# Kernel tuning notes

Hardware: AMD Instinct MI355X
Metric: run time of the kernel (lower is better)

Reference implementation:

```python
import jax, jax.numpy as jnp
import numpy as np

B, TOPK, E, C, K = 64, 2, 16, 1024, 4096


def setup_inputs() -> dict:
    key = jax.random.key(0)
    k1, k2, k3, k4, k5, k6 = jax.random.split(key, 6)
    return {
        "activated": jax.random.normal(k1, (B, TOPK, K), dtype=jnp.float32),
        "expert_indices": jax.random.randint(k2, (B, TOPK), 0, E, dtype=jnp.int64)
        if jax.config.jax_enable_x64 else jax.random.randint(k2, (B, TOPK), 0, E, dtype=jnp.int32),
        "expert_weights": jax.random.uniform(k3, (B, TOPK), dtype=jnp.float32),
        "mlp2_weight": jax.random.normal(k4, (E, C, K), dtype=jnp.float32),
        "mlp2_bias": jax.random.normal(k5, (E, C), dtype=jnp.float32),
        "residual_x": jax.random.normal(k6, (B, C), dtype=jnp.float32),
    }


def reference(activated, expert_indices, expert_weights, mlp2_weight, mlp2_bias, residual_x):
    # Gather per-token expert weights/biases: w [B, topk, C, K], b [B, topk, C]
    w = mlp2_weight[expert_indices]
    b = mlp2_bias[expert_indices]
    # Batched matvec per (token, expert slot): t [B, topk, C]
    t = jnp.einsum("beck,bek->bec", w, activated) + b
    # Weighted combine over top-k expert slots, plus residual: [B, C]
    return residual_x + jnp.einsum("bec,be->bc", t, expert_weights)
```

## Files before the change

### kernel.cpp

```cpp
#include <hip/hip_runtime.h>

#define BB    64
#define TOPK  2
#define EE    16
#define CC    1024
#define KK    4096

constexpr int RPB = 8;
constexpr int P   = 16;
constexpr int NW  = KK / 4 / 64;

__global__ __launch_bounds__(256) void route_init(
    const int* __restrict__ idx, const float* __restrict__ ew,
    const float* __restrict__ bias, const float* __restrict__ resid,
    float* __restrict__ out, int* __restrict__ cnt, int* __restrict__ lists)
{
    if (blockIdx.x == 0) {
        __shared__ int scnt[EE];
        if (threadIdx.x < EE) scnt[threadIdx.x] = 0;
        __syncthreads();
        if (threadIdx.x < BB * TOPK) {
            int e = idx[threadIdx.x];
            int pos = atomicAdd(&scnt[e], 1);
            lists[e * 128 + pos] = threadIdx.x;
        }
        __syncthreads();
        if (threadIdx.x < EE) cnt[threadIdx.x] = scnt[threadIdx.x];
    } else {
        int i = (blockIdx.x - 1) * 256 + threadIdx.x;
        int b = i >> 10;
        int c = i & (CC - 1);
        float v = resid[i];
#pragma unroll
        for (int s = 0; s < TOPK; s++) {
            int e = idx[b * TOPK + s];
            v += ew[b * TOPK + s] * bias[e * CC + c];
        }
        out[i] = v;
    }
}

__global__ __launch_bounds__(256) void moe_mlp2(
    const float* __restrict__ act, const float* __restrict__ ew,
    const float* __restrict__ W, float* __restrict__ out,
    const int* __restrict__ cnt, const int* __restrict__ lists)
{
    const int e = blockIdx.x >> 7;
    const int n = cnt[e];
    if (n == 0) return;
    const int c0   = (blockIdx.x & 127) * RPB;
    const int lane = threadIdx.x & 63;
    const int wave = threadIdx.x >> 6;
    const float4* We0 = (const float4*)(W + (size_t)(e * CC + c0 + wave * 2) * KK);
    const float4* We1 = We0 + (KK / 4);

    for (int g = 0; g < n; g += P) {
        const int np = min(P, n - g);

        int aoff[P];
#pragma unroll
        for (int p = 0; p < P; p++)
            aoff[p] = (p < np) ? lists[e * 128 + g + p] * (KK * 4) : 0;

        float acc[2][P];
#pragma unroll
        for (int r = 0; r < 2; r++)
#pragma unroll
            for (int p = 0; p < P; p++) acc[r][p] = 0.f;

#pragma unroll 2
        for (int kw = 0; kw < NW; kw++) {
            const int fi = kw * 64 + lane;
            const float4 w0 = We0[fi];
            const float4 w1 = We1[fi];
            const char* abase = (const char*)act + ((size_t)fi << 4);
#pragma unroll
            for (int pc = 0; pc < P / 4; pc++) {
                if (pc * 4 < np) {
#pragma unroll
                    for (int j = 0; j < 4; j++) {
                        const int p = pc * 4 + j;
                        const float4 a = *(const float4*)(abase + aoff[p]);
                        acc[0][p] += w0.x * a.x + w0.y * a.y + w0.z * a.z + w0.w * a.w;
                        acc[1][p] += w1.x * a.x + w1.y * a.y + w1.z * a.z + w1.w * a.w;
                    }
                }
            }
        }

#pragma unroll
        for (int p = 0; p < P; p++) {
            if (p < np) {
                float v0 = acc[0][p];
                float v1 = acc[1][p];
#pragma unroll
                for (int off = 32; off > 0; off >>= 1) {
                    v0 += __shfl_down(v0, off, 64);
                    v1 += __shfl_down(v1, off, 64);
                }
                if (lane == 0) {
                    int pr = lists[e * 128 + g + p];
                    float w = ew[pr];
                    float* o = out + (pr >> 1) * CC + c0 + wave * 2;
                    atomicAdd(o + 0, w * v0);
                    atomicAdd(o + 1, w * v1);
                }
            }
        }
    }
}

extern "C" void kernel_launch(void* const* d_in, const int* in_sizes, int n_in,
                              void* d_out, int out_size, void* d_ws, size_t ws_size,
                              hipStream_t stream) {
    const float* act   = (const float*)d_in[0];
    const int*   idx   = (const int*)d_in[1];
    const float* ew    = (const float*)d_in[2];
    const float* W     = (const float*)d_in[3];
    const float* bias  = (const float*)d_in[4];
    const float* resid = (const float*)d_in[5];
    float* out = (float*)d_out;

    int* cnt   = (int*)d_ws;
    int* lists = (int*)d_ws + 64;

    route_init<<<1 + (BB * CC) / 256, 256, 0, stream>>>(
        idx, ew, bias, resid, out, cnt, lists);
    moe_mlp2<<<EE * (CC / RPB), 256, 0, stream>>>(
        act, ew, W, out, cnt, lists);
}
```

Before: 404.6 us.

## Process four rows per wave, split K across two blocks, use nontemporal weight loads

Each wave now computes four weight rows instead of two, so every activation float4 load is reused across twice as many rows. The K dimension is split in half across paired blocks, which keeps the same grid size while doubling rows per block. Weight loads use nontemporal hints because the weight stream is read once. In exchange, register pressure from a 4x16 accumulator array rises, and there are twice as many atomic adds into the output.

```diff
diff --git a/kernel.cpp b/kernel.cpp
--- a/kernel.cpp
+++ b/kernel.cpp
@@ -6,9 +6,13 @@
 #define CC    1024
 #define KK    4096
 
-constexpr int RPB = 8;
+constexpr int RPB = 16;
 constexpr int P   = 16;
-constexpr int NW  = KK / 4 / 64;
+constexpr int KS  = 2;
+constexpr int KH  = KK / KS;
+constexpr int NW  = KH / 4 / 64;
+
+typedef float v4f __attribute__((ext_vector_type(4)));
 
 __global__ __launch_bounds__(256) void route_init(
     const int* __restrict__ idx, const float* __restrict__ ew,
@@ -45,44 +49,56 @@
     const float* __restrict__ W, float* __restrict__ out,
     const int* __restrict__ cnt, const int* __restrict__ lists)
 {
-    const int e = blockIdx.x >> 7;
+    const int bid = blockIdx.x;
+    const int e = bid >> 7;
     const int n = cnt[e];
     if (n == 0) return;
-    const int c0   = (blockIdx.x & 127) * RPB;
+    const int ct = (bid >> 1) & 63;
+    const int ks = bid & 1;
+    const int c0   = ct * RPB;
     const int lane = threadIdx.x & 63;
     const int wave = threadIdx.x >> 6;
-    const float4* We0 = (const float4*)(W + (size_t)(e * CC + c0 + wave * 2) * KK);
-    const float4* We1 = We0 + (KK / 4);
+    const int row0 = c0 + wave * 4;
+    const v4f* __restrict__ Wb =
+        (const v4f*)(W + (size_t)(e * CC + row0) * KK + ks * KH);
+    const char* __restrict__ actb = (const char*)(act + ks * KH);
 
     for (int g = 0; g < n; g += P) {
         const int np = min(P, n - g);
 
         int aoff[P];
+        int pid[P];
 #pragma unroll
-        for (int p = 0; p < P; p++)
-            aoff[p] = (p < np) ? lists[e * 128 + g + p] * (KK * 4) : 0;
+        for (int p = 0; p < P; p++) {
+            pid[p]  = (p < np) ? lists[e * 128 + g + p] : 0;
+            aoff[p] = pid[p] * (KK * 4);
+        }
 
-        float acc[2][P];
+        float acc[4][P];
 #pragma unroll
-        for (int r = 0; r < 2; r++)
+        for (int r = 0; r < 4; r++)
 #pragma unroll
             for (int p = 0; p < P; p++) acc[r][p] = 0.f;
 
 #pragma unroll 2
         for (int kw = 0; kw < NW; kw++) {
             const int fi = kw * 64 + lane;
-            const float4 w0 = We0[fi];
-            const float4 w1 = We1[fi];
-            const char* abase = (const char*)act + ((size_t)fi << 4);
+            v4f w4[4];
+#pragma unroll
+            for (int r = 0; r < 4; r++)
+                w4[r] = __builtin_nontemporal_load(Wb + (size_t)r * (KK / 4) + fi);
+            const char* abase = actb + ((size_t)fi << 4);
 #pragma unroll
             for (int pc = 0; pc < P / 4; pc++) {
                 if (pc * 4 < np) {
 #pragma unroll
                     for (int j = 0; j < 4; j++) {
                         const int p = pc * 4 + j;
-                        const float4 a = *(const float4*)(abase + aoff[p]);
-                        acc[0][p] += w0.x * a.x + w0.y * a.y + w0.z * a.z + w0.w * a.w;
-                        acc[1][p] += w1.x * a.x + w1.y * a.y + w1.z * a.z + w1.w * a.w;
+                        const v4f a = *(const v4f*)(abase + aoff[p]);
+#pragma unroll
+                        for (int r = 0; r < 4; r++)
+                            acc[r][p] += w4[r].x * a.x + w4[r].y * a.y +
+                                         w4[r].z * a.z + w4[r].w * a.w;
                     }
                 }
             }
@@ -91,19 +107,23 @@
 #pragma unroll
         for (int p = 0; p < P; p++) {
             if (p < np) {
-                float v0 = acc[0][p];
-                float v1 = acc[1][p];
+                float v0 = acc[0][p], v1 = acc[1][p];
+                float v2 = acc[2][p], v3 = acc[3][p];
 #pragma unroll
                 for (int off = 32; off > 0; off >>= 1) {
                     v0 += __shfl_down(v0, off, 64);
                     v1 += __shfl_down(v1, off, 64);
+                    v2 += __shfl_down(v2, off, 64);
+                    v3 += __shfl_down(v3, off, 64);
                 }
                 if (lane == 0) {
-                    int pr = lists[e * 128 + g + p];
+                    int pr = pid[p];
                     float w = ew[pr];
-                    float* o = out + (pr >> 1) * CC + c0 + wave * 2;
+                    float* o = out + (pr >> 1) * CC + row0;
                     atomicAdd(o + 0, w * v0);
                     atomicAdd(o + 1, w * v1);
+                    atomicAdd(o + 2, w * v2);
+                    atomicAdd(o + 3, w * v3);
                 }
             }
         }
@@ -126,6 +146,6 @@
 
     route_init<<<1 + (BB * CC) / 256, 256, 0, stream>>>(
         idx, ew, bias, resid, out, cnt, lists);
-    moe_mlp2<<<EE * (CC / RPB), 256, 0, stream>>>(
+    moe_mlp2<<<EE * (CC / RPB) * KS, 256, 0, stream>>>(
         act, ew, W, out, cnt, lists);
 }
```

Result: no change. 397.4 us (-1.8%).
